# Performance work log

Measured on AMD Instinct MI355X. Metric: run time of the kernel, lower is better.

## Reference

```python
import jax, jax.numpy as jnp
import numpy as np

D = 768
B, T = 4, 4096


def _layernorm(x, gamma, bias):
    # Faithful to the (buggy) original: (x - mu/sqrt(var)) * gamma + bias,
    # with torch's default unbiased variance (ddof=1).
    mu = jnp.mean(x, axis=-1, keepdims=True)
    var = jnp.var(x, axis=-1, keepdims=True, ddof=1)
    return (x - mu / jnp.sqrt(var)) * gamma + bias


def setup_inputs() -> dict:
    key = jax.random.key(0)
    ks = jax.random.split(key, 8)
    # kaiming_uniform_ default: bound = sqrt(6 / fan_in) with a=sqrt(5) -> gain = sqrt(2/(1+5)) = sqrt(1/3)
    # bound = gain * sqrt(3/fan_in) = sqrt(1/fan_in)
    bound_attn = 1.0 / np.sqrt(D)
    bound_lin = 1.0 / np.sqrt(D)  # torch Linear default init bound
    return {
        "x": jax.random.normal(ks[0], (B, T, D), dtype=jnp.float32),
        "ln1_g": jnp.ones((D,), jnp.float32),
        "ln1_b": jnp.zeros((D,), jnp.float32),
        "wq": jax.random.uniform(ks[1], (D, D), jnp.float32, -bound_attn, bound_attn),
        "wk": jax.random.uniform(ks[2], (D, D), jnp.float32, -bound_attn, bound_attn),
        "wv": jax.random.uniform(ks[3], (D, D), jnp.float32, -bound_attn, bound_attn),
        "ln2_g": jnp.ones((D,), jnp.float32),
        "ln2_b": jnp.zeros((D,), jnp.float32),
        "fc1_w": jax.random.uniform(ks[4], (D, D), jnp.float32, -bound_lin, bound_lin),
        "fc1_b": jax.random.uniform(ks[5], (D,), jnp.float32, -bound_lin, bound_lin),
        "fc2_w": jax.random.uniform(ks[6], (D, D), jnp.float32, -bound_lin, bound_lin),
        "fc2_b": jax.random.uniform(ks[7], (D,), jnp.float32, -bound_lin, bound_lin),
    }


def reference(x, ln1_g, ln1_b, wq, wk, wv, ln2_g, ln2_b, fc1_w, fc1_b, fc2_w, fc2_b):
    d_model = x.shape[-1]
    # LN 1
    y = _layernorm(x, ln1_g, ln1_b)
    # Naive single-head attention (no causal mask, scale 1/sqrt(d_model))
    q = jnp.einsum("btk,kd->btd", y, wq)
    k = jnp.einsum("btk,kd->btd", y, wk)
    v = jnp.einsum("btk,kd->btd", y, wv)
    scale = 1.0 / jnp.sqrt(jnp.asarray(d_model, y.dtype))
    a = jax.nn.softmax(jnp.einsum("bqd,bkd->bqk", q, k) * scale, axis=-1)
    y = jnp.einsum("bqt,btd->bqd", a, v)
    # LN 2
    y = _layernorm(y, ln2_g, ln2_b)
    # MLP: Linear -> ReLU -> Linear (Dropout in eval mode = identity)
    h = jax.nn.relu(jnp.einsum("btd,od->bto", y, fc1_w) + fc1_b)
    y = jnp.einsum("btd,od->bto", h, fc2_w) + fc2_b
    # Residual
    return x + y
```

## Files before the change

kernel.cpp:

```cpp
#include <hip/hip_runtime.h>
#include <hip/hip_bf16.h>


#define DDIM 768
#define TT   4096
#define NB   4
#define ROWS (NB * TT)

using bf16 = __hip_bfloat16;
typedef __bf16 bf16x8 __attribute__((ext_vector_type(8)));
typedef float  f32x4  __attribute__((ext_vector_type(4)));
typedef unsigned short us4 __attribute__((ext_vector_type(4)));

__device__ __forceinline__ float to_f(float x) { return x; }
__device__ __forceinline__ float to_f(bf16 x) { return __bfloat162float(x); }

__device__ __forceinline__ unsigned short bfb(float f) {
  bf16 b = __float2bfloat16(f);
  return __builtin_bit_cast(unsigned short, b);
}

__device__ __forceinline__ void gload16(const void* g, void* l) {
#if __has_builtin(__builtin_amdgcn_global_load_lds)
  __builtin_amdgcn_global_load_lds(
      (const __attribute__((address_space(1))) void*)g,
      (__attribute__((address_space(3))) void*)l, 16, 0, 0);
#else
  int lane = threadIdx.x & 63;
  ((int4*)l)[lane] = *(const int4*)g;
#endif
}

template <int MODE, int SWZ, int NT, int MT>
__global__ __launch_bounds__(256) void gemm_bt(
    const bf16* __restrict__ A, int lda, long sA,
    const bf16* __restrict__ B, int ldb, long sB,
    void* __restrict__ Cout, int ldc, long sC, int K, float scale,
    const float* __restrict__ bias, const float* __restrict__ resid,
    float* __restrict__ Lsum) {
  __shared__ __align__(16) bf16 As[128 * 64];
  __shared__ __align__(16) bf16 Bs[128 * 64];
  __shared__ float Lred[128];

  int bx, by, bz;
  if constexpr (SWZ == 1) {
    const int h   = blockIdx.x;
    const int xcd = h & 7;
    const int s   = h >> 3;
    bx = s % NT;
    const int g = (s / NT) * 8 + xcd;
    by = g % MT;
    bz = g / MT;
  } else if constexpr (SWZ == 2) {
    const int h   = blockIdx.x;
    const int xcd = h & 7;
    const int s   = h >> 3;
    by = s % MT;
    const int g = (s / MT) * 8 + xcd;
    bx = g % NT;
    bz = g / NT;
  } else {
    bx = blockIdx.x; by = blockIdx.y; bz = blockIdx.z;
  }

  int kz = 0;
  if constexpr (MODE == 7) { kz = bz >> 2; bz &= 3; }

  A += (long)bz * sA + (long)kz * 2048;
  B += (long)bz * sB + (long)kz * 2048;

  const int tid  = threadIdx.x;
  const int wave = tid >> 6;
  const int lane = tid & 63;
  const int l16  = lane & 15;
  const int lq   = lane >> 4;
  const int wm   = wave >> 1;
  const int wn   = wave & 1;
  const long tileM = (long)by * 128;
  const long tileN = (long)bx * 128;

  if constexpr (MODE == 5) {
    if (tid < 128) Lred[tid] = 0.f;
  }

  f32x4 acc[4][4] = {};

  unsigned int aoff[4], boff[4];
#pragma unroll
  for (int q = 0; q < 4; ++q) {
    const int p    = (q * 4 + wave) * 1024 + lane * 16;
    const int lg   = p ^ (((p >> 7) & 7) << 4);
    const int row  = lg >> 7;
    const int colb = lg & 127;
    aoff[q] = (unsigned int)((tileM + row) * (long)lda * 2 + colb);
    boff[q] = (unsigned int)((tileN + row) * (long)ldb * 2 + colb);
  }

  const char* Ab = (const char*)A;
  const char* Bb = (const char*)B;
  char* AsB = (char*)As;
  char* BsB = (char*)Bs;
  const int sw = (l16 & 7) << 4;

  for (int kb = 0; kb < K * 2; kb += 128) {
#pragma unroll
    for (int q = 0; q < 4; ++q)
      gload16(Ab + (aoff[q] + kb), AsB + (q * 4 + wave) * 1024);
#pragma unroll
    for (int q = 0; q < 4; ++q)
      gload16(Bb + (boff[q] + kb), BsB + (q * 4 + wave) * 1024);
    __syncthreads();

#pragma unroll
    for (int kk = 0; kk < 2; ++kk) {
      bf16x8 af[4], bf_[4];
      const int ks = (kk * 64 + lq * 16) ^ sw;
#pragma unroll
      for (int i = 0; i < 4; ++i)
        af[i] = *(const bf16x8*)(AsB + (wm * 64 + i * 16 + l16) * 128 + ks);
#pragma unroll
      for (int j = 0; j < 4; ++j)
        bf_[j] = *(const bf16x8*)(BsB + (wn * 64 + j * 16 + l16) * 128 + ks);
#pragma unroll
      for (int i = 0; i < 4; ++i)
#pragma unroll
        for (int j = 0; j < 4; ++j)
          acc[i][j] = __builtin_amdgcn_mfma_f32_16x16x32_bf16(af[i], bf_[j],
                                                              acc[i][j], 0, 0, 0);
    }
    __syncthreads();
  }

  const long base_m = tileM + wm * 64;
  const long base_n = tileN + wn * 64;

  if constexpr (MODE == 5) {
    bf16* P = (bf16*)Cout + (long)bz * sC;
    float ps[4] = {0.f, 0.f, 0.f, 0.f};
#pragma unroll
    for (int j = 0; j < 4; ++j) {
      const long colq = base_n + j * 16 + l16;
#pragma unroll
      for (int i = 0; i < 4; ++i) {
        const long krow = base_m + i * 16 + lq * 4;
        const float p0 = exp2f(acc[i][j][0] * scale);
        const float p1 = exp2f(acc[i][j][1] * scale);
        const float p2 = exp2f(acc[i][j][2] * scale);
        const float p3 = exp2f(acc[i][j][3] * scale);
        ps[j] += (p0 + p1) + (p2 + p3);
        us4 w = {bfb(p0), bfb(p1), bfb(p2), bfb(p3)};
        *(us4*)(P + colq * (long)ldc + krow) = w;
      }
    }
#pragma unroll
    for (int j = 0; j < 4; ++j) {
      float v = ps[j];
      v += __shfl_xor(v, 16);
      v += __shfl_xor(v, 32);
      if (lq == 0) atomicAdd(&Lred[wn * 64 + j * 16 + l16], v);
    }
    __syncthreads();
    if (tid < 128) atomicAdd(&Lsum[(long)bz * TT + tileN + tid], Lred[tid]);
  } else if constexpr (MODE == 7) {
    bf16* Op = (bf16*)Cout + (long)kz * ((long)ROWS * DDIM) + (long)bz * sC;
#pragma unroll
    for (int j = 0; j < 4; ++j) {
      const long colq = base_n + j * 16 + l16;
#pragma unroll
      for (int i = 0; i < 4; ++i) {
        const long drow = base_m + i * 16 + lq * 4;
        us4 w = {bfb(acc[i][j][0]), bfb(acc[i][j][1]),
                 bfb(acc[i][j][2]), bfb(acc[i][j][3])};
        *(us4*)(Op + colq * (long)ldc + drow) = w;
      }
    }
  } else if constexpr (MODE == 3) {
    bf16* Hp = (bf16*)Cout;
#pragma unroll
    for (int i = 0; i < 4; ++i) {
      const long drow = base_m + i * 16 + lq * 4;
      const f32x4 bv = *(const f32x4*)&bias[drow];
#pragma unroll
      for (int j = 0; j < 4; ++j) {
        const long colt = base_n + j * 16 + l16;
        float v0 = acc[i][j][0] + bv[0]; v0 = v0 > 0.f ? v0 : 0.f;
        float v1 = acc[i][j][1] + bv[1]; v1 = v1 > 0.f ? v1 : 0.f;
        float v2 = acc[i][j][2] + bv[2]; v2 = v2 > 0.f ? v2 : 0.f;
        float v3 = acc[i][j][3] + bv[3]; v3 = v3 > 0.f ? v3 : 0.f;
        us4 w = {bfb(v0), bfb(v1), bfb(v2), bfb(v3)};
        *(us4*)(Hp + colt * (long)ldc + drow) = w;
      }
    }
  } else {
    float* Op = (float*)Cout;
#pragma unroll
    for (int i = 0; i < 4; ++i) {
      const long drow = base_m + i * 16 + lq * 4;
      const f32x4 bv = *(const f32x4*)&bias[drow];
#pragma unroll
      for (int j = 0; j < 4; ++j) {
        const long off = (base_n + j * 16 + l16) * (long)ldc + drow;
        const f32x4 rs = *(const f32x4*)&resid[off];
        f32x4 o;
        o[0] = acc[i][j][0] + bv[0] + rs[0];
        o[1] = acc[i][j][1] + bv[1] + rs[1];
        o[2] = acc[i][j][2] + bv[2] + rs[2];
        o[3] = acc[i][j][3] + bv[3] + rs[3];
        __builtin_nontemporal_store(o, (f32x4*)(Op + off));
      }
    }
  }
}

__global__ __launch_bounds__(256) void gemm_qkv(
    const bf16* __restrict__ Y,
    const bf16* __restrict__ Wq, const bf16* __restrict__ Wk,
    const bf16* __restrict__ Wv, bf16* __restrict__ Qm,
    bf16* __restrict__ Km, bf16* __restrict__ Vt) {
  __shared__ __align__(16) bf16 As[128 * 64];
  __shared__ __align__(16) bf16 Bs[128 * 64];

  const int z = blockIdx.z;
  const bf16* Ap = (z == 2) ? Wv : Y;
  const bf16* Bp = (z == 0) ? Wq : (z == 1) ? Wk : Y;

  const int tid  = threadIdx.x;
  const int wave = tid >> 6;
  const int lane = tid & 63;
  const int l16  = lane & 15;
  const int lq   = lane >> 4;
  const int wm   = wave >> 1;
  const int wn   = wave & 1;
  const long tileM = (z == 2) ? (long)blockIdx.x * 128 : (long)blockIdx.y * 128;
  const long tileN = (z == 2) ? (long)blockIdx.y * 128 : (long)blockIdx.x * 128;

  unsigned int aoff[4], boff[4];
#pragma unroll
  for (int q = 0; q < 4; ++q) {
    const int p    = (q * 4 + wave) * 1024 + lane * 16;
    const int lg   = p ^ (((p >> 7) & 7) << 4);
    const int row  = lg >> 7;
    const int colb = lg & 127;
    aoff[q] = (unsigned int)((tileM + row) * (long)DDIM * 2 + colb);
    boff[q] = (unsigned int)((tileN + row) * (long)DDIM * 2 + colb);
  }

  f32x4 acc[4][4] = {};

  const char* Ab = (const char*)Ap;
  const char* Bb = (const char*)Bp;
  char* AsB = (char*)As;
  char* BsB = (char*)Bs;
  const int sw = (l16 & 7) << 4;

  for (int kb = 0; kb < DDIM * 2; kb += 128) {
#pragma unroll
    for (int q = 0; q < 4; ++q)
      gload16(Ab + (aoff[q] + kb), AsB + (q * 4 + wave) * 1024);
#pragma unroll
    for (int q = 0; q < 4; ++q)
      gload16(Bb + (boff[q] + kb), BsB + (q * 4 + wave) * 1024);
    __syncthreads();

#pragma unroll
    for (int kk = 0; kk < 2; ++kk) {
      bf16x8 af[4], bf_[4];
      const int ks = (kk * 64 + lq * 16) ^ sw;
#pragma unroll
      for (int i = 0; i < 4; ++i)
        af[i] = *(const bf16x8*)(AsB + (wm * 64 + i * 16 + l16) * 128 + ks);
#pragma unroll
      for (int j = 0; j < 4; ++j)
        bf_[j] = *(const bf16x8*)(BsB + (wn * 64 + j * 16 + l16) * 128 + ks);
#pragma unroll
      for (int i = 0; i < 4; ++i)
#pragma unroll
        for (int j = 0; j < 4; ++j)
          acc[i][j] = __builtin_amdgcn_mfma_f32_16x16x32_bf16(af[i], bf_[j],
                                                              acc[i][j], 0, 0, 0);
    }
    __syncthreads();
  }

  const long base_m = tileM + wm * 64;
  const long base_n = tileN + wn * 64;
  bf16* Cp = (z == 0) ? Qm : (z == 1) ? Km : Vt;
  const long ldo = (z < 2) ? (long)DDIM : (long)ROWS;
#pragma unroll
  for (int i = 0; i < 4; ++i)
#pragma unroll
    for (int j = 0; j < 4; ++j)
#pragma unroll
      for (int r = 0; r < 4; ++r) {
        const long row = base_m + i * 16 + lq * 4 + r;
        const long col = base_n + j * 16 + l16;
        Cp[row * ldo + col] = __float2bfloat16(acc[i][j][r]);
      }
}

template <typename T, int DUAL>
__global__ __launch_bounds__(256) void ln_kernel(
    const T* __restrict__ in, const T* __restrict__ in2,
    const float* __restrict__ Ldiv, const float* __restrict__ g,
    const float* __restrict__ beta, bf16* __restrict__ out,
    float* __restrict__ Lzero) {
  const long row = blockIdx.x;
  if (Lzero != nullptr && threadIdx.x == 0) Lzero[row] = 0.f;
  const T* xr = in + row * DDIM;
  const int t = threadIdx.x;
  float v0 = to_f(xr[t]), v1 = to_f(xr[t + 256]), v2 = to_f(xr[t + 512]);
  if constexpr (DUAL) {
    const T* xr2 = in2 + row * DDIM;
    v0 += to_f(xr2[t]); v1 += to_f(xr2[t + 256]); v2 += to_f(xr2[t + 512]);
    const float invL = 1.0f / Ldiv[row];
    v0 *= invL; v1 *= invL; v2 *= invL;
  }
  float s = v0 + v1 + v2;
  float q = v0 * v0 + v1 * v1 + v2 * v2;
#pragma unroll
  for (int o = 32; o; o >>= 1) {
    s += __shfl_down(s, o);
    q += __shfl_down(q, o);
  }
  __shared__ float sb[4], qb[4];
  if ((t & 63) == 0) { sb[t >> 6] = s; qb[t >> 6] = q; }
  __syncthreads();
  const float S = sb[0] + sb[1] + sb[2] + sb[3];
  const float Q = qb[0] + qb[1] + qb[2] + qb[3];
  const float mu  = S * (1.0f / 768.0f);
  const float var = (Q - 768.0f * mu * mu) * (1.0f / 767.0f);
  const float sub = mu / sqrtf(var);
  bf16* orow = out + row * DDIM;
  orow[t]       = __float2bfloat16((v0 - sub) * g[t]       + beta[t]);
  orow[t + 256] = __float2bfloat16((v1 - sub) * g[t + 256] + beta[t + 256]);
  orow[t + 512] = __float2bfloat16((v2 - sub) * g[t + 512] + beta[t + 512]);
}

__global__ void prep_weights(const float* __restrict__ wq,
                             const float* __restrict__ wk,
                             const float* __restrict__ wv,
                             const float* __restrict__ f1,
                             const float* __restrict__ f2,
                             bf16* wqt, bf16* wkt, bf16* wvt, bf16* f1b,
                             bf16* f2b) {
  __shared__ float tile[32][33];
  const float* src;
  bf16* dst;
  bool tr = true;
  switch (blockIdx.z) {
    case 0: src = wq; dst = wqt; break;
    case 1: src = wk; dst = wkt; break;
    case 2: src = wv; dst = wvt; break;
    case 3: src = f1; dst = f1b; tr = false; break;
    default: src = f2; dst = f2b; tr = false; break;
  }
  const int tx = threadIdx.x, ty = threadIdx.y;
  const int x = blockIdx.x * 32 + tx;
  const int y = blockIdx.y * 32 + ty;
  if (tr) {
#pragma unroll
    for (int r = 0; r < 4; ++r) tile[ty + 8 * r][tx] = src[(y + 8 * r) * DDIM + x];
    __syncthreads();
    const int ox = blockIdx.y * 32 + tx;
    const int oy = blockIdx.x * 32 + ty;
#pragma unroll
    for (int r = 0; r < 4; ++r)
      dst[(oy + 8 * r) * DDIM + ox] = __float2bfloat16(tile[tx][ty + 8 * r]);
  } else {
#pragma unroll
    for (int r = 0; r < 4; ++r)
      dst[(y + 8 * r) * DDIM + x] = __float2bfloat16(src[(y + 8 * r) * DDIM + x]);
  }
}

extern "C" void kernel_launch(void* const* d_in, const int* in_sizes, int n_in,
                              void* d_out, int out_size, void* d_ws,
                              size_t ws_size, hipStream_t stream) {
  const float* x     = (const float*)d_in[0];
  const float* ln1_g = (const float*)d_in[1];
  const float* ln1_b = (const float*)d_in[2];
  const float* wq    = (const float*)d_in[3];
  const float* wk    = (const float*)d_in[4];
  const float* wv    = (const float*)d_in[5];
  const float* ln2_g = (const float*)d_in[6];
  const float* ln2_b = (const float*)d_in[7];
  const float* f1w   = (const float*)d_in[8];
  const float* f1bias= (const float*)d_in[9];
  const float* f2w   = (const float*)d_in[10];
  const float* f2bias= (const float*)d_in[11];
  float* out = (float*)d_out;

  char* ws = (char*)d_ws;
  size_t off = 0;
  auto take = [&](size_t bytes) -> char* {
    char* p = ws + off;
    off += (bytes + 255) & ~(size_t)255;
    return p;
  };
  const size_t WB = (size_t)DDIM * DDIM * sizeof(bf16);
  const size_t MB = (size_t)ROWS * DDIM * sizeof(bf16);
  bf16* wqt = (bf16*)take(WB);
  bf16* wkt = (bf16*)take(WB);
  bf16* wvt = (bf16*)take(WB);
  bf16* f1b = (bf16*)take(WB);
  bf16* f2b = (bf16*)take(WB);
  float* Lsum = (float*)take((size_t)ROWS * sizeof(float));
  bf16* y1  = (bf16*)take(MB);
  bf16* Qm  = (bf16*)take(MB);
  bf16* Km  = (bf16*)take(MB);
  bf16* Vt  = (bf16*)take(MB);
  bf16* Sb  = (bf16*)take((size_t)NB * TT * TT * sizeof(bf16));
  bf16* O0 = y1;
  bf16* O1 = Qm;
  bf16* y2 = Km;
  bf16* h  = y1;

  prep_weights<<<dim3(24, 24, 5), dim3(32, 8), 0, stream>>>(
      wq, wk, wv, f1w, f2w, wqt, wkt, wvt, f1b, f2b);

  ln_kernel<float, 0><<<ROWS, 256, 0, stream>>>(x, nullptr, nullptr, ln1_g,
                                                ln1_b, y1, Lsum);

  gemm_qkv<<<dim3(6, 128, 3), 256, 0, stream>>>(y1, wqt, wkt, wvt, Qm, Km, Vt);

  const float scale2 = 0.03608439182435161f * 1.4426950408889634f;
  gemm_bt<5, 1, 32, 32><<<dim3(32 * 32 * NB), 256, 0, stream>>>(
      Km, DDIM, (long)TT * DDIM, Qm, DDIM, (long)TT * DDIM, Sb, TT,
      (long)TT * TT, DDIM, scale2, nullptr, nullptr, Lsum);

  gemm_bt<7, 2, 32, 6><<<dim3(6 * 32 * NB * 2), 256, 0, stream>>>(
      Vt, ROWS, (long)TT, Sb, TT, (long)TT * TT, O0, DDIM, (long)TT * DDIM,
      TT / 2, 1.f, nullptr, nullptr, nullptr);

  ln_kernel<bf16, 1><<<ROWS, 256, 0, stream>>>(O0, O1, Lsum, ln2_g, ln2_b, y2,
                                               nullptr);

  gemm_bt<3, 2, 128, 6><<<dim3(128 * 6), 256, 0, stream>>>(
      f1b, DDIM, 0, y2, DDIM, 0, h, DDIM, 0, DDIM, 1.f, f1bias, nullptr,
      nullptr);
  gemm_bt<4, 2, 128, 6><<<dim3(128 * 6), 256, 0, stream>>>(
      f2b, DDIM, 0, h, DDIM, 0, out, DDIM, 0, DDIM, 1.f, f2bias, x, nullptr);
}
```

Baseline: 566.9 us.

## Replace QK^T score GEMM with 256x256 double-buffered 8-wave pipelined kernel

Adds a dedicated 512-thread kernel for the attention score GEMM. It uses 256x256 tiles, double-buffered LDS staging with explicit vmcnt waits and barriers, and interleaves MFMA quadrants with LDS reads and global prefetches. The exp2 and row-sum epilogue moves into this kernel, and the old MODE 5 path is removed from the generic GEMM. The larger tiles raise data reuse and the pipeline is meant to hide load latency. In exchange the kernel uses heavy register and LDS footprints (64 KB per block), which lowers occupancy.

```diff
diff --git a/kernel.cpp b/kernel.cpp
--- a/kernel.cpp
+++ b/kernel.cpp
@@ -31,6 +31,198 @@
 #endif
 }
 
+#define SBAR()                                        \
+  do {                                                \
+    __builtin_amdgcn_sched_barrier(0);                \
+    asm volatile("s_barrier" ::: "memory");           \
+    __builtin_amdgcn_sched_barrier(0);                \
+  } while (0)
+#define VMW8() asm volatile("s_waitcnt vmcnt(8)" ::: "memory")
+#define VMW0() asm volatile("s_waitcnt vmcnt(0)" ::: "memory")
+
+template <int IH, int JH>
+__device__ __forceinline__ void mmaQ(f32x4 (&acc)[8][4],
+                                     const bf16x8 (&af)[4][2],
+                                     const bf16x8 (&bfh)[2][2]) {
+  __builtin_amdgcn_s_setprio(1);
+#pragma unroll
+  for (int ii = 0; ii < 4; ++ii)
+#pragma unroll
+    for (int jj = 0; jj < 2; ++jj)
+#pragma unroll
+      for (int kk = 0; kk < 2; ++kk)
+        acc[IH * 4 + ii][JH * 2 + jj] = __builtin_amdgcn_mfma_f32_16x16x32_bf16(
+            af[ii][kk], bfh[jj][kk], acc[IH * 4 + ii][JH * 2 + jj], 0, 0, 0);
+  __builtin_amdgcn_s_setprio(0);
+}
+
+__global__ __launch_bounds__(512) void gemm_qk8(
+    const bf16* __restrict__ A, int lda, long sA,
+    const bf16* __restrict__ B, int ldb, long sB,
+    bf16* __restrict__ Pout, int ldc, long sC, int K, float scale,
+    float* __restrict__ Lsum) {
+  __shared__ __align__(16) bf16 As[2][256 * 64];
+  __shared__ __align__(16) bf16 Bs[2][256 * 64];
+
+  const int h   = blockIdx.x;
+  const int xcd = h & 7;
+  const int s   = h >> 3;
+  const int bx  = s % 16;
+  const int g   = (s / 16) * 8 + xcd;
+  const int by  = g % 16;
+  const int bz  = g / 16;
+
+  const char* Ab = (const char*)(A + (long)bz * sA);
+  const char* Bb = (const char*)(B + (long)bz * sB);
+
+  const int tid  = threadIdx.x;
+  const int wave = tid >> 6;
+  const int lane = tid & 63;
+  const int l16  = lane & 15;
+  const int lq   = lane >> 4;
+  const int wm   = wave >> 2;
+  const int wn   = wave & 3;
+  const long tileM = (long)by * 256;
+  const long tileN = (long)bx * 256;
+
+  const int  pu  = wave * 1024 + lane * 16;
+  const int  r0  = pu >> 7;
+  const int  cc0 = (pu & 127) ^ ((r0 & 7) << 4);
+  const long aoff   = (tileM + r0) * (long)lda * 2 + cc0;
+  const long boff   = (tileN + r0) * (long)ldb * 2 + cc0;
+  const long arow64 = 64 * (long)lda * 2;
+  const long brow64 = 64 * (long)ldb * 2;
+  char* As0 = (char*)As[0];
+  char* As1 = (char*)As[1];
+  char* Bs0 = (char*)Bs[0];
+  char* Bs1 = (char*)Bs[1];
+  const int ldst = wave * 1024;
+
+  auto stageA = [&](char* dst, int t) {
+    const long kb = (long)t * 128;
+    gload16(Ab + aoff + kb,               dst + ldst);
+    gload16(Ab + aoff + arow64 + kb,      dst + 8192 + ldst);
+    gload16(Ab + aoff + 2 * arow64 + kb,  dst + 16384 + ldst);
+    gload16(Ab + aoff + 3 * arow64 + kb,  dst + 24576 + ldst);
+  };
+  auto stageB = [&](char* dst, int t) {
+    const long kb = (long)t * 128;
+    gload16(Bb + boff + kb,               dst + ldst);
+    gload16(Bb + boff + brow64 + kb,      dst + 8192 + ldst);
+    gload16(Bb + boff + 2 * brow64 + kb,  dst + 16384 + ldst);
+    gload16(Bb + boff + 3 * brow64 + kb,  dst + 24576 + ldst);
+  };
+
+  const int sw = (l16 & 7) << 4;
+  auto rdA = [&](const char* buf, int ih, bf16x8 (&af)[4][2]) {
+#pragma unroll
+    for (int ii = 0; ii < 4; ++ii)
+#pragma unroll
+      for (int kk = 0; kk < 2; ++kk)
+        af[ii][kk] = *(const bf16x8*)(buf +
+            (wm * 128 + ih * 64 + ii * 16 + l16) * 128 +
+            ((kk * 64 + lq * 16) ^ sw));
+  };
+  auto rdB = [&](const char* buf, int jh, bf16x8 (&bfh)[2][2]) {
+#pragma unroll
+    for (int jj = 0; jj < 2; ++jj)
+#pragma unroll
+      for (int kk = 0; kk < 2; ++kk)
+        bfh[jj][kk] = *(const bf16x8*)(buf +
+            (wn * 64 + (jh * 2 + jj) * 16 + l16) * 128 +
+            ((kk * 64 + lq * 16) ^ sw));
+  };
+
+  f32x4 acc[8][4] = {};
+  bf16x8 af[4][2], bf0[2][2], bf1[2][2];
+
+  stageA(As0, 0);
+  stageB(Bs0, 0);
+  stageA(As1, 1);
+
+  const int NI = K / 128;
+  for (int I = 0; I < NI; ++I) {
+    const int a = 2 * I, b = 2 * I + 1;
+    const bool last = (I == NI - 1);
+
+    stageB(Bs1, b);
+    VMW8();
+    SBAR();
+    rdA(As0, 0, af);
+    rdB(Bs0, 0, bf0);
+    mmaQ<0, 0>(acc, af, bf0);
+    SBAR();
+    rdB(Bs0, 1, bf1);
+    SBAR();
+    mmaQ<0, 1>(acc, af, bf1);
+    SBAR();
+    rdA(As0, 1, af);
+    SBAR();
+    mmaQ<1, 1>(acc, af, bf1);
+    SBAR();
+    if (!last) stageA(As0, a + 2);
+    SBAR();
+    mmaQ<1, 0>(acc, af, bf0);
+    SBAR();
+
+    if (!last) {
+      stageB(Bs0, a + 2);
+      VMW8();
+    } else {
+      VMW0();
+    }
+    SBAR();
+    rdA(As1, 0, af);
+    rdB(Bs1, 0, bf0);
+    mmaQ<0, 0>(acc, af, bf0);
+    SBAR();
+    rdB(Bs1, 1, bf1);
+    SBAR();
+    mmaQ<0, 1>(acc, af, bf1);
+    SBAR();
+    rdA(As1, 1, af);
+    SBAR();
+    mmaQ<1, 1>(acc, af, bf1);
+    SBAR();
+    if (!last) stageA(As1, b + 2);
+    SBAR();
+    mmaQ<1, 0>(acc, af, bf0);
+    SBAR();
+  }
+
+  float* Lred = (float*)As0;
+  const long base_k = tileM + wm * 128;
+  const long base_q = tileN + wn * 64;
+  bf16* P = Pout + (long)bz * sC;
+  float ps[4] = {0.f, 0.f, 0.f, 0.f};
+#pragma unroll
+  for (int j = 0; j < 4; ++j) {
+    const long colq = base_q + j * 16 + l16;
+#pragma unroll
+    for (int i = 0; i < 8; ++i) {
+      const long krow = base_k + i * 16 + lq * 4;
+      const float p0 = exp2f(acc[i][j][0] * scale);
+      const float p1 = exp2f(acc[i][j][1] * scale);
+      const float p2 = exp2f(acc[i][j][2] * scale);
+      const float p3 = exp2f(acc[i][j][3] * scale);
+      ps[j] += (p0 + p1) + (p2 + p3);
+      us4 w = {bfb(p0), bfb(p1), bfb(p2), bfb(p3)};
+      *(us4*)(P + colq * (long)ldc + krow) = w;
+    }
+  }
+  if (tid < 256) Lred[tid] = 0.f;
+  __syncthreads();
+#pragma unroll
+  for (int j = 0; j < 4; ++j) {
+    float v = ps[j];
+    v += __shfl_xor(v, 16);
+    v += __shfl_xor(v, 32);
+    if (lq == 0) atomicAdd(&Lred[wn * 64 + j * 16 + l16], v);
+  }
+  __syncthreads();
+  if (tid < 256) atomicAdd(&Lsum[(long)bz * TT + tileN + tid], Lred[tid]);
+}
+
 template <int MODE, int SWZ, int NT, int MT>
 __global__ __launch_bounds__(256) void gemm_bt(
     const bf16* __restrict__ A, int lda, long sA,
@@ -40,7 +232,6 @@
     float* __restrict__ Lsum) {
   __shared__ __align__(16) bf16 As[128 * 64];
   __shared__ __align__(16) bf16 Bs[128 * 64];
-  __shared__ float Lred[128];
 
   int bx, by, bz;
   if constexpr (SWZ == 1) {
@@ -79,10 +270,6 @@
   const long tileM = (long)by * 128;
   const long tileN = (long)bx * 128;
 
-  if constexpr (MODE == 5) {
-    if (tid < 128) Lred[tid] = 0.f;
-  }
-
   f32x4 acc[4][4] = {};
 
   unsigned int aoff[4], boff[4];
@@ -134,34 +321,7 @@
   const long base_m = tileM + wm * 64;
   const long base_n = tileN + wn * 64;
 
-  if constexpr (MODE == 5) {
-    bf16* P = (bf16*)Cout + (long)bz * sC;
-    float ps[4] = {0.f, 0.f, 0.f, 0.f};
-#pragma unroll
-    for (int j = 0; j < 4; ++j) {
-      const long colq = base_n + j * 16 + l16;
-#pragma unroll
-      for (int i = 0; i < 4; ++i) {
-        const long krow = base_m + i * 16 + lq * 4;
-        const float p0 = exp2f(acc[i][j][0] * scale);
-        const float p1 = exp2f(acc[i][j][1] * scale);
-        const float p2 = exp2f(acc[i][j][2] * scale);
-        const float p3 = exp2f(acc[i][j][3] * scale);
-        ps[j] += (p0 + p1) + (p2 + p3);
-        us4 w = {bfb(p0), bfb(p1), bfb(p2), bfb(p3)};
-        *(us4*)(P + colq * (long)ldc + krow) = w;
-      }
-    }
-#pragma unroll
-    for (int j = 0; j < 4; ++j) {
-      float v = ps[j];
-      v += __shfl_xor(v, 16);
-      v += __shfl_xor(v, 32);
-      if (lq == 0) atomicAdd(&Lred[wn * 64 + j * 16 + l16], v);
-    }
-    __syncthreads();
-    if (tid < 128) atomicAdd(&Lsum[(long)bz * TT + tileN + tid], Lred[tid]);
-  } else if constexpr (MODE == 7) {
+  if constexpr (MODE == 7) {
     bf16* Op = (bf16*)Cout + (long)kz * ((long)ROWS * DDIM) + (long)bz * sC;
 #pragma unroll
     for (int j = 0; j < 4; ++j) {
@@ -424,9 +584,9 @@
   gemm_qkv<<<dim3(6, 128, 3), 256, 0, stream>>>(y1, wqt, wkt, wvt, Qm, Km, Vt);
 
   const float scale2 = 0.03608439182435161f * 1.4426950408889634f;
-  gemm_bt<5, 1, 32, 32><<<dim3(32 * 32 * NB), 256, 0, stream>>>(
+  gemm_qk8<<<dim3(16 * 16 * NB), 512, 0, stream>>>(
       Km, DDIM, (long)TT * DDIM, Qm, DDIM, (long)TT * DDIM, Sb, TT,
-      (long)TT * TT, DDIM, scale2, nullptr, nullptr, Lsum);
+      (long)TT * TT, DDIM, scale2, Lsum);
 
   gemm_bt<7, 2, 32, 6><<<dim3(6 * 32 * NB * 2), 256, 0, stream>>>(
       Vt, ROWS, (long)TT, Sb, TT, (long)TT * TT, O0, DDIM, (long)TT * DDIM,
```

After: 549.8 us. 1.03x faster.
